# Optimization experiments

Hardware: AMD Instinct MI355X
Metric: run time of the kernel (lower is better)

## Reference

```python
import jax, jax.numpy as jnp
import numpy as np

D_MODEL = 512
D_STATE = 16
D_INNER = 2 * D_MODEL  # expand_factor=2
IN_CH = 256
B_SZ, H_SZ, W_SZ = 4, 32, 32


def setup_inputs() -> dict:
    key = jax.random.key(0)
    ks = jax.random.split(key, 24)
    f = jax.random.normal
    inp = {}
    inp["x_V"] = f(ks[0], (B_SZ, IN_CH, H_SZ, W_SZ), jnp.float32)
    inp["x_I"] = f(ks[1], (B_SZ, IN_CH, H_SZ, W_SZ), jnp.float32)
    # channel_reduce: 1x1 conv + BN (inference stats)
    inp["conv_red_w"] = f(ks[2], (D_MODEL, IN_CH), jnp.float32) * 0.05
    inp["bn_red_g"] = jnp.ones((D_MODEL,), jnp.float32)
    inp["bn_red_b"] = jnp.zeros((D_MODEL,), jnp.float32)
    inp["bn_red_m"] = jnp.zeros((D_MODEL,), jnp.float32)
    inp["bn_red_v"] = jnp.ones((D_MODEL,), jnp.float32)
    # channel_restore: 1x1 conv + BN
    inp["conv_res_w"] = f(ks[3], (IN_CH, D_MODEL), jnp.float32) * 0.05
    inp["bn_res_g"] = jnp.ones((IN_CH,), jnp.float32)
    inp["bn_res_b"] = jnp.zeros((IN_CH,), jnp.float32)
    inp["bn_res_m"] = jnp.zeros((IN_CH,), jnp.float32)
    inp["bn_res_v"] = jnp.ones((IN_CH,), jnp.float32)
    # lambda_predictor convs (1x1 on pooled features == linear)
    inp["lam_w1"] = f(ks[4], (D_MODEL // 4, D_MODEL * 2), jnp.float32) * 0.05
    inp["lam_b1"] = jnp.zeros((D_MODEL // 4,), jnp.float32)
    inp["lam_w2"] = f(ks[5], (2, D_MODEL // 4), jnp.float32) * 0.05
    inp["lam_b2"] = jnp.zeros((2,), jnp.float32)
    # two SimplifiedMamba2Blocks
    for i, p in enumerate(["V", "I"]):
        kk = jax.random.split(ks[6 + i], 6)
        inp[p + "_in_w"] = f(kk[0], (2 * D_INNER, D_MODEL), jnp.float32) * 0.03
        inp[p + "_out_w"] = f(kk[1], (D_MODEL, D_INNER), jnp.float32) * 0.03
        # A = -exp(A_log) in (-1, -0.05): stable decay
        inp[p + "_A_log"] = jnp.log(jax.random.uniform(kk[2], (D_INNER, D_STATE), jnp.float32, 0.05, 0.95))
        inp[p + "_B"] = f(kk[3], (D_INNER, D_STATE), jnp.float32) * 0.05
        inp[p + "_C"] = jnp.full((D_INNER, D_STATE), 0.01, jnp.float32)
        inp[p + "_ln_g"] = jnp.ones((D_MODEL,), jnp.float32)
        inp[p + "_ln_b"] = jnp.zeros((D_MODEL,), jnp.float32)
    inp["gate"] = jnp.asarray(0.1, jnp.float32)
    return inp


def _bn(x, g, b, m, v):
    # x: (B,C,H,W); inference-mode batchnorm
    return (x - m[:, None, None]) / jnp.sqrt(v[:, None, None] + 1e-5) * g[:, None, None] + b[:, None, None]


def _conv1x1(x, w):
    return jnp.einsum('bchw,oc->bohw', x, w)


def _ssm_scan(x_ssm, A, Bm, Cm, reverse):
    # x_ssm: (B,L,I); A,Bm,Cm: (I,S)
    bsz = x_ssm.shape[0]
    h0 = jnp.zeros((bsz, A.shape[0], A.shape[1]), x_ssm.dtype)

    def step(h, xt):  # xt: (B,I)
        h = jnp.clip(h * A + xt[:, :, None] * Bm, -10.0, 10.0)
        return h, jnp.einsum('bis,is->bi', h, Cm)

    _, ys = jax.lax.scan(step, h0, jnp.swapaxes(x_ssm, 0, 1), reverse=reverse)
    return jnp.swapaxes(ys, 0, 1)  # (B,L,I), in original time order


def _mamba(x, ln_g, ln_b, in_w, out_w, A_log, Bm, Cm):
    # LayerNorm
    mu = jnp.mean(x, -1, keepdims=True)
    var = jnp.mean((x - mu) ** 2, -1, keepdims=True)
    xn = (x - mu) / jnp.sqrt(var + 1e-5) * ln_g + ln_b
    xp = xn @ in_w.T  # (B,L,2*I)
    x_ssm, gate = jnp.split(xp, 2, axis=-1)
    A = jnp.clip(-jnp.exp(A_log), -10.0, -0.01)
    yf = _ssm_scan(x_ssm, A, Bm, Cm, False)
    yb = _ssm_scan(x_ssm, A, Bm, Cm, True)
    out = 0.5 * (yf + yb) * jax.nn.silu(gate)
    return out @ out_w.T


def reference(x_V, x_I, conv_red_w, bn_red_g, bn_red_b, bn_red_m, bn_red_v,
              conv_res_w, bn_res_g, bn_res_b, bn_res_m, bn_res_v,
              lam_w1, lam_b1, lam_w2, lam_b2,
              V_in_w, V_out_w, V_A_log, V_B, V_C, V_ln_g, V_ln_b,
              I_in_w, I_out_w, I_A_log, I_B, I_C, I_ln_g, I_ln_b, gate):
    B, _, H, W = x_V.shape
    xVr = jax.nn.relu(_bn(_conv1x1(x_V, conv_red_w), bn_red_g, bn_red_b, bn_red_m, bn_red_v))
    xIr = jax.nn.relu(_bn(_conv1x1(x_I, conv_red_w), bn_red_g, bn_red_b, bn_red_m, bn_red_v))
    # same spatial size -> adaptive pooling and [:B] slicing are identities
    conc = jnp.concatenate([xVr, xIr], axis=1)  # (B, 2*d_model, H, W)

    def lam(c):
        p = jnp.mean(c, axis=(2, 3))  # global avg pool -> (B, 2*d_model)
        h1 = jax.nn.relu(p @ lam_w1.T + lam_b1)
        return jax.nn.softmax(h1 @ lam_w2.T + lam_b2, axis=-1)  # (B,2)

    lamV = lam(conc)
    lamI = lam(conc)

    seq_V = jnp.swapaxes(xVr.reshape(B, D_MODEL, H * W), 1, 2)  # (B,L,D)
    seq_I = jnp.swapaxes(xIr.reshape(B, D_MODEL, H * W), 1, 2)

    outV_std = _mamba(seq_V, V_ln_g, V_ln_b, V_in_w, V_out_w, V_A_log, V_B, V_C)
    outI_std = _mamba(seq_I, I_ln_g, I_ln_b, I_in_w, I_out_w, I_A_log, I_B, I_C)
    outV_cross = _mamba(seq_V, V_ln_g, V_ln_b, V_in_w, V_out_w, V_A_log, jax.lax.stop_gradient(I_B), V_C)
    outI_cross = _mamba(seq_I, I_ln_g, I_ln_b, I_in_w, I_out_w, I_A_log, jax.lax.stop_gradient(V_B), I_C)

    outV = lamV[:, 0][:, None, None] * outV_std + lamV[:, 1][:, None, None] * outV_cross
    outI = lamI[:, 0][:, None, None] * outI_std + lamI[:, 1][:, None, None] * outI_cross

    featV = jnp.swapaxes(outV, 1, 2).reshape(B, D_MODEL, H, W)
    featI = jnp.swapaxes(outI, 1, 2).reshape(B, D_MODEL, H, W)
    featV = _bn(_conv1x1(featV, conv_res_w), bn_res_g, bn_res_b, bn_res_m, bn_res_v)
    featI = _bn(_conv1x1(featI, conv_res_w), bn_res_g, bn_res_b, bn_res_m, bn_res_v)

    g = jax.nn.sigmoid(gate)
    return (x_V + g * featV, x_I + g * featI)
```

## Files before the change

### kernel.cpp

```cpp
#include <hip/hip_runtime.h>
#include <hip/hip_bf16.h>
#include <math.h>

#define L_SZ 1024
#define DM   512
#define DI   1024
#define NS   16
#define CH   256

typedef float4 f4;
typedef __attribute__((ext_vector_type(8))) short short8;
typedef __attribute__((ext_vector_type(4))) float f32x4;

__device__ __forceinline__ float bf2f(ushort u) {
    union { unsigned int i; float f; } x; x.i = ((unsigned int)u) << 16; return x.f;
}
__device__ __forceinline__ ushort f2bf(float f) {
    union { float f; unsigned int i; } x; x.f = f;
    unsigned int r = x.i + 0x7FFFu + ((x.i >> 16) & 1u);
    return (ushort)(r >> 16);
}
__device__ __forceinline__ uint pkbf(float a, float b) {
    union { __hip_bfloat162 h; uint u; } c;
    c.h = __float22bfloat162_rn(make_float2(a, b));
    return c.u;
}

#define GLOAD16(gp, lp) \
  __builtin_amdgcn_global_load_lds((const __attribute__((address_space(1))) void*)(gp), \
                                   (__attribute__((address_space(3))) void*)(lp), 16, 0, 0)

__global__ __launch_bounds__(256) void k_cast_all(
    const float* __restrict__ s0, const float* __restrict__ s1,
    const float* __restrict__ s2, const float* __restrict__ s3,
    const float* __restrict__ s4, const float* __restrict__ s5,
    ushort* __restrict__ d0, ushort* __restrict__ d1,
    ushort* __restrict__ d2, ushort* __restrict__ d3,
    ushort* __restrict__ d4, ushort* __restrict__ d5)
{
    const int bid = blockIdx.x;
    const float* s; ushort* d; int rel;
    if      (bid < 128)  { s = s0; d = d0; rel = bid; }
    else if (bid < 256)  { s = s1; d = d1; rel = bid - 128; }
    else if (bid < 1280) { s = s2; d = d2; rel = bid - 256; }
    else if (bid < 2304) { s = s3; d = d3; rel = bid - 1280; }
    else if (bid < 2816) { s = s4; d = d4; rel = bid - 2304; }
    else                 { s = s5; d = d5; rel = bid - 2816; }
    const int i = rel * 256 + threadIdx.x;
    f4 v = ((const f4*)s)[i];
    ushort4 o;
    o.x = f2bf(v.x); o.y = f2bf(v.y); o.z = f2bf(v.z); o.w = f2bf(v.w);
    ((ushort4*)d)[i] = o;
}

__global__ __launch_bounds__(256) void k_xt(const float* __restrict__ xv,
                                            const float* __restrict__ xi,
                                            ushort* __restrict__ xtv,
                                            ushort* __restrict__ xti)
{
    __shared__ float tile[32][36];
    const int t = threadIdx.x;
    const int l0 = blockIdx.x * 32, c0 = blockIdx.y * 32;
    const int b = blockIdx.z & 3, st = blockIdx.z >> 2;
    const float* x = st ? xi : xv;
    ushort* xt = st ? xti : xtv;
    {
        int cc = t >> 3, ll4 = (t & 7) << 2;
        f4 v = *(const f4*)(x + ((size_t)(b * CH + c0 + cc)) * L_SZ + l0 + ll4);
        tile[cc][ll4 + 0] = v.x; tile[cc][ll4 + 1] = v.y;
        tile[cc][ll4 + 2] = v.z; tile[cc][ll4 + 3] = v.w;
    }
    __syncthreads();
    {
        int ll = t >> 3, cc4 = (t & 7) << 2;
        ushort4 o;
        o.x = f2bf(tile[cc4 + 0][ll]); o.y = f2bf(tile[cc4 + 1][ll]);
        o.z = f2bf(tile[cc4 + 2][ll]); o.w = f2bf(tile[cc4 + 3][ll]);
        *(ushort4*)(xt + ((size_t)(b * L_SZ + l0 + ll)) * CH + c0 + cc4) = o;
    }
}

template<int MODE, int BM, int BN>
__global__ __launch_bounds__(256) void k_gemm(
    const ushort* __restrict__ A0, const ushort* __restrict__ A1,
    const ushort* __restrict__ B0, const ushort* __restrict__ B1,
    int K,
    float* __restrict__ o0, float* __restrict__ o1,
    ushort* __restrict__ ob0, ushort* __restrict__ ob1,
    ushort* __restrict__ sb0, ushort* __restrict__ sb1,
    const float* __restrict__ pg, const float* __restrict__ pb,
    const float* __restrict__ pm, const float* __restrict__ pv,
    const float* __restrict__ x0, const float* __restrict__ x1,
    const float* __restrict__ gate, float* __restrict__ pp)
{
    constexpr int MT   = BM / 32;
    constexpr int NT   = BN / 32;
    constexpr int ASEG = BM / 16;
    constexpr int NSEG = (BM + BN) / 16;
    constexpr int SPW  = NSEG / 4;
    __shared__ __align__(16) ushort Sl[(BM + BN) * 32];
    const int t = threadIdx.x;
    const int wv = t >> 6, lane = t & 63;
    const int n0 = blockIdx.x * BN, m0 = blockIdx.y * BM;
    const int st = blockIdx.z;
    const ushort* Ap = st ? A1 : A0;
    const ushort* Bp = st ? B1 : B0;
    const int wm = wv >> 1, wn = wv & 1;
    const int lrow = lane & 15, q = lane >> 4;
    f32x4 acc[MT][NT];
    #pragma unroll
    for (int a_ = 0; a_ < MT; ++a_)
        #pragma unroll
        for (int b_ = 0; b_ < NT; ++b_)
            acc[a_][b_] = (f32x4){0.f, 0.f, 0.f, 0.f};
    const int srow = lane >> 2;
    const int skk  = (((lane & 3) ^ ((lane >> 3) & 3)) << 3);
    const int koff = ((q ^ ((lrow >> 1) & 3)) << 3);
    for (int k0 = 0; k0 < K; k0 += 32) {
        #pragma unroll
        for (int s2 = 0; s2 < SPW; ++s2) {
            const int seg = wv * SPW + s2;
            const int grow = (seg < ASEG) ? (m0 + seg * 16 + srow)
                                          : (n0 + (seg - ASEG) * 16 + srow);
            const ushort* src = (seg < ASEG) ? Ap : Bp;
            GLOAD16(src + (size_t)grow * K + k0 + skk, &Sl[seg * 512]);
        }
        __syncthreads();
        short8 af[MT], bfr[NT];
        #pragma unroll
        for (int mt = 0; mt < MT; ++mt)
            af[mt] = *(const short8*)&Sl[(wm * (MT * 16) + mt * 16 + lrow) * 32 + koff];
        #pragma unroll
        for (int nt = 0; nt < NT; ++nt)
            bfr[nt] = *(const short8*)&Sl[(BM + wn * (NT * 16) + nt * 16 + lrow) * 32 + koff];
        #pragma unroll
        for (int mt = 0; mt < MT; ++mt)
            #pragma unroll
            for (int nt = 0; nt < NT; ++nt)
                acc[mt][nt] = __builtin_amdgcn_mfma_f32_16x16x32_bf16(af[mt], bfr[nt], acc[mt][nt], 0, 0, 0);
        __syncthreads();
    }
    if (MODE == 0) {
        float* op = st ? o1 : o0;
        const int b = m0 >> 10;
        #pragma unroll
        for (int nt = 0; nt < NT; ++nt) {
            const int gn = n0 + wn * (NT * 16) + nt * 16 + lrow;
            const float s  = pg[gn] * rsqrtf(pv[gn] + 1e-5f);
            const float sh = pb[gn] - pm[gn] * s;
            float psum = 0.f;
            #pragma unroll
            for (int mt = 0; mt < MT; ++mt) {
                const int gm = m0 + wm * (MT * 16) + mt * 16 + q * 4;
                #pragma unroll
                for (int r = 0; r < 4; ++r) {
                    const float v = fmaxf(fmaf(acc[mt][nt][r], s, sh), 0.f);
                    op[(size_t)(gm + r) * DM + gn] = v;
                    psum += v;
                }
            }
            psum += __shfl_xor(psum, 16, 64);
            psum += __shfl_xor(psum, 32, 64);
            if (q == 0)
                atomicAdd(pp + (b * 1024 + st * 512 + gn), psum * (1.0f / 1024.0f));
        }
    } else if (MODE == 1) {
        const bool isx = (n0 < 1024);
        ushort* xp = st ? ob1 : ob0;
        ushort* sp = st ? sb1 : sb0;
        #pragma unroll
        for (int nt = 0; nt < NT; ++nt) {
            const int gn = n0 + wn * (NT * 16) + nt * 16 + lrow;
            #pragma unroll
            for (int mt = 0; mt < MT; ++mt) {
                const int gm = m0 + wm * (MT * 16) + mt * 16 + q * 4;
                if (isx) {
                    const uint u01 = pkbf(acc[mt][nt][0], acc[mt][nt][1]);
                    const uint u23 = pkbf(acc[mt][nt][2], acc[mt][nt][3]);
                    ushort* bp = xp + (size_t)gm * DI + gn;
                    bp[0]      = (ushort)u01;
                    bp[DI]     = (ushort)(u01 >> 16);
                    bp[2 * DI] = (ushort)u23;
                    bp[3 * DI] = (ushort)(u23 >> 16);
                } else {
                    float sv[4];
                    #pragma unroll
                    for (int r = 0; r < 4; ++r) {
                        const float v = acc[mt][nt][r];
                        sv[r] = v / (1.f + __expf(-v));
                    }
                    const uint u01 = pkbf(sv[0], sv[1]);
                    const uint u23 = pkbf(sv[2], sv[3]);
                    ushort* bp = sp + (size_t)gm * DI + gn - 1024;
                    bp[0]      = (ushort)u01;
                    bp[DI]     = (ushort)(u01 >> 16);
                    bp[2 * DI] = (ushort)u23;
                    bp[3 * DI] = (ushort)(u23 >> 16);
                }
            }
        }
    } else if (MODE == 2) {
        ushort* fp_ = st ? ob1 : ob0;
        #pragma unroll
        for (int nt = 0; nt < NT; ++nt) {
            const int gn = n0 + wn * (NT * 16) + nt * 16 + lrow;
            #pragma unroll
            for (int mt = 0; mt < MT; ++mt) {
                const int gm = m0 + wm * (MT * 16) + mt * 16 + q * 4;
                const uint u01 = pkbf(acc[mt][nt][0], acc[mt][nt][1]);
                const uint u23 = pkbf(acc[mt][nt][2], acc[mt][nt][3]);
                ushort* bp = fp_ + (size_t)gm * DM + gn;
                bp[0]      = (ushort)u01;
                bp[DM]     = (ushort)(u01 >> 16);
                bp[2 * DM] = (ushort)u23;
                bp[3 * DM] = (ushort)(u23 >> 16);
            }
        }
    } else {
        const float* xin = st ? x1 : x0;
        float* op = st ? o1 : o0;
        const float g = 1.f / (1.f + __expf(-gate[0]));
        #pragma unroll
        for (int nt = 0; nt < NT; ++nt) {
            const int gn = n0 + wn * (NT * 16) + nt * 16 + lrow;
            const float s  = pg[gn] * rsqrtf(pv[gn] + 1e-5f);
            const float sh = pb[gn] - pm[gn] * s;
            #pragma unroll
            for (int mt = 0; mt < MT; ++mt) {
                const int gmb = m0 + wm * (MT * 16) + mt * 16 + q * 4;
                const int b = gmb >> 10, l = gmb & 1023;
                const size_t off = ((size_t)(b * CH + gn)) * L_SZ + l;
                f4 xi = *(const f4*)(xin + off);
                f4 o;
                o.x = xi.x + g * fmaf(acc[mt][nt][0], s, sh);
                o.y = xi.y + g * fmaf(acc[mt][nt][1], s, sh);
                o.z = xi.z + g * fmaf(acc[mt][nt][2], s, sh);
                o.w = xi.w + g * fmaf(acc[mt][nt][3], s, sh);
                *(f4*)(op + off) = o;
            }
        }
    }
}

__global__ __launch_bounds__(256) void k_lam1(
    const float* __restrict__ p, const float* __restrict__ w1,
    const float* __restrict__ b1, float* __restrict__ h1)
{
    const int t = threadIdx.x, lane = t & 63, wv = t >> 6;
    const int idx = blockIdx.x * 4 + wv;
    const int b = idx >> 7, j = idx & 127;
    const float* pb = p + b * 1024;
    const float* wr = w1 + j * 1024;
    float s = 0.f;
    #pragma unroll
    for (int k = 0; k < 16; ++k)
        s = fmaf(pb[lane + k * 64], wr[lane + k * 64], s);
    #pragma unroll
    for (int off = 1; off < 64; off <<= 1) s += __shfl_xor(s, off, 64);
    if (lane == 0) h1[idx] = fmaxf(s + b1[j], 0.f);
}

__global__ __launch_bounds__(512) void k_lam2(
    const float* __restrict__ h1, const float* __restrict__ w2,
    const float* __restrict__ b2, float* __restrict__ lam)
{
    __shared__ float lg[8];
    const int t = threadIdx.x, lane = t & 63, wv = t >> 6;
    const int b = wv >> 1, k = wv & 1;
    const float* hb = h1 + b * 128;
    const float* wr = w2 + k * 128;
    float s = fmaf(hb[lane], wr[lane], hb[lane + 64] * wr[lane + 64]);
    #pragma unroll
    for (int off = 1; off < 64; off <<= 1) s += __shfl_xor(s, off, 64);
    if (lane == 0) lg[wv] = s + b2[k];
    __syncthreads();
    if (t < 4) {
        const float a0 = lg[t * 2], a1 = lg[t * 2 + 1];
        const float m  = fmaxf(a0, a1);
        const float e0 = __expf(a0 - m), e1 = __expf(a1 - m);
        const float inv = 1.f / (e0 + e1);
        lam[t * 2 + 0] = e0 * inv;
        lam[t * 2 + 1] = e1 * inv;
    }
}

__global__ __launch_bounds__(128) void k_ln(
    const float* __restrict__ seq0, const float* __restrict__ seq1,
    const float* __restrict__ g0, const float* __restrict__ b0,
    const float* __restrict__ g1, const float* __restrict__ b1,
    ushort* __restrict__ ln0, ushort* __restrict__ ln1)
{
    __shared__ float red[2][2];
    const int row = blockIdx.x, st = blockIdx.y;
    const float* seq = st ? seq1 : seq0;
    const float* gg  = st ? g1 : g0;
    const float* bb  = st ? b1 : b0;
    ushort* ln = st ? ln1 : ln0;
    const int t = threadIdx.x, wv2 = t >> 6, lane = t & 63;
    f4 v = *(const f4*)(seq + (size_t)row * DM + t * 4);
    float s = v.x + v.y + v.z + v.w;
    float ss = v.x * v.x + v.y * v.y + v.z * v.z + v.w * v.w;
    #pragma unroll
    for (int off = 1; off < 64; off <<= 1) {
        s += __shfl_xor(s, off, 64); ss += __shfl_xor(ss, off, 64);
    }
    if (lane == 0) { red[wv2][0] = s; red[wv2][1] = ss; }
    __syncthreads();
    const float tot = red[0][0] + red[1][0], tot2 = red[0][1] + red[1][1];
    const float mu = tot * (1.f / 512.f);
    const float rstd = rsqrtf(tot2 * (1.f / 512.f) - mu * mu + 1e-5f);
    f4 gv = *(const f4*)(gg + t * 4);
    f4 bv = *(const f4*)(bb + t * 4);
    ushort4 o;
    o.x = f2bf(fmaf((v.x - mu) * rstd, gv.x, bv.x));
    o.y = f2bf(fmaf((v.y - mu) * rstd, gv.y, bv.y));
    o.z = f2bf(fmaf((v.z - mu) * rstd, gv.z, bv.z));
    o.w = f2bf(fmaf((v.w - mu) * rstd, gv.w, bv.w));
    *(ushort4*)(ln + (size_t)row * DM + t * 4) = o;
}

__global__ __launch_bounds__(256) void k_scan(
    const ushort* __restrict__ xsV, const ushort* __restrict__ xsI,
    const float* __restrict__ VA, const float* __restrict__ VB,
    const float* __restrict__ VC, const float* __restrict__ IA,
    const float* __restrict__ IB, const float* __restrict__ IC,
    const float* __restrict__ lam,
    ushort* __restrict__ accfV, ushort* __restrict__ accbV,
    ushort* __restrict__ accfI, ushort* __restrict__ accbI)
{
    __shared__ __align__(16) ushort xbuf[2][32][128];
    const int t = threadIdx.x;
    const int lane = t & 63, wv = t >> 6;
    const int shalf = t & 1;
    const int il = t >> 1;
    const int b = blockIdx.y;
    const int cfg = blockIdx.z & 3, j = blockIdx.z >> 2;
    const int st = cfg >> 1, dir = cfg & 1;
    const ushort* xs = st ? xsI : xsV;
    const float* Alog = st ? IA : VA;
    const float* Cm   = st ? IC : VC;
    const float* Bown = st ? IB : VB;
    const float* Both = st ? VB : IB;
    ushort* out = st ? (dir ? accbI : accfI) : (dir ? accbV : accfV);
    const float lam0 = lam[b * 2 + 0], lam1 = lam[b * 2 + 1];
    float a[8], w[8], g[8];
    const int base = (blockIdx.x * 128 + il) * NS + shalf * 8;
    #pragma unroll
    for (int s = 0; s < 8; ++s) {
        a[s] = fminf(fmaxf(-__expf(Alog[base + s]), -10.f), -0.01f);
        w[s] = Cm[base + s] * fmaf(lam0, Bown[base + s], lam1 * Both[base + s]);
        g[s] = 0.f;
    }
    const ushort* xbase = xs + (size_t)b * L_SZ * DI + blockIdx.x * 128;
    ushort* op = out + (size_t)b * L_SZ * DI + blockIdx.x * 128 + il;
    const int c0    = j == 0 ? 0 : 4 * j - 3;
    const int ncha  = j == 0 ? 4 : 7;
    const int nwarm = j == 0 ? 0 : 3;
    const int lrow  = wv * 4 + (lane >> 4);
    const int lcol8 = (lane & 15) << 3;
    {
        #pragma unroll
        for (int is = 0; is < 2; ++is) {
            const int lr = (c0 << 5) + is * 16 + lrow;
            const int l  = dir ? (1023 - lr) : lr;
            GLOAD16(xbase + (size_t)l * DI + lcol8, &xbuf[0][is * 16 + wv * 4][0]);
        }
    }
    __syncthreads();
    for (int ci = 0; ci < ncha; ++ci) {
        const int cidx = c0 + ci;
        const int buf = ci & 1;
        if (ci + 1 < ncha) {
            #pragma unroll
            for (int is = 0; is < 2; ++is) {
                const int lr = ((cidx + 1) << 5) + is * 16 + lrow;
                const int l  = dir ? (1023 - lr) : lr;
                GLOAD16(xbase + (size_t)l * DI + lcol8, &xbuf[buf ^ 1][is * 16 + wv * 4][0]);
            }
        }
        if (ci < nwarm) {
            #pragma unroll
            for (int n = 0; n < 32; ++n) {
                const float x = bf2f(xbuf[buf][n][il]);
                #pragma unroll
                for (int s = 0; s < 8; ++s)
                    g[s] = fmaf(a[s], g[s], x);
            }
        } else {
            #pragma unroll
            for (int n = 0; n < 32; ++n) {
                const float x = bf2f(xbuf[buf][n][il]);
                float y0 = 0.f, y1 = 0.f;
                #pragma unroll
                for (int s = 0; s < 8; s += 2) {
                    g[s]     = fmaf(a[s],     g[s],     x);
                    y0       = fmaf(g[s],     w[s],     y0);
                    g[s + 1] = fmaf(a[s + 1], g[s + 1], x);
                    y1       = fmaf(g[s + 1], w[s + 1], y1);
                }
                float z = y0 + y1;
                z += __shfl_xor(z, 1, 64);
                if (shalf == 0) {
                    const int lp = (cidx << 5) + n;
                    const int l  = dir ? (1023 - lp) : lp;
                    op[(size_t)l * DI] = f2bf(z);
                }
            }
        }
        __syncthreads();
    }
}

__global__ __launch_bounds__(256) void k_combine(
    const ushort* __restrict__ fV, const ushort* __restrict__ bV,
    const ushort* __restrict__ fI, const ushort* __restrict__ bI,
    const ushort* __restrict__ sgV, const ushort* __restrict__ sgI,
    ushort* __restrict__ yV, ushort* __restrict__ yI)
{
    const int st = blockIdx.y;
    const size_t i = (size_t)blockIdx.x * 256 + threadIdx.x;
    const ushort4 f = ((const ushort4*)(st ? fI : fV))[i];
    const ushort4 g = ((const ushort4*)(st ? bI : bV))[i];
    const ushort4 s = ((const ushort4*)(st ? sgI : sgV))[i];
    ushort4 o;
    o.x = f2bf((bf2f(f.x) + bf2f(g.x)) * 0.5f * bf2f(s.x));
    o.y = f2bf((bf2f(f.y) + bf2f(g.y)) * 0.5f * bf2f(s.y));
    o.z = f2bf((bf2f(f.z) + bf2f(g.z)) * 0.5f * bf2f(s.z));
    o.w = f2bf((bf2f(f.w) + bf2f(g.w)) * 0.5f * bf2f(s.w));
    ((ushort4*)(st ? yI : yV))[i] = o;
}

extern "C" void kernel_launch(void* const* d_in, const int* in_sizes, int n_in,
                              void* d_out, int out_size, void* d_ws, size_t ws_size,
                              hipStream_t stream)
{
    const float* xV       = (const float*)d_in[0];
    const float* xI       = (const float*)d_in[1];
    const float* convredw = (const float*)d_in[2];
    const float* bnredg   = (const float*)d_in[3];
    const float* bnredb   = (const float*)d_in[4];
    const float* bnredm   = (const float*)d_in[5];
    const float* bnredv   = (const float*)d_in[6];
    const float* convresw = (const float*)d_in[7];
    const float* bnresg   = (const float*)d_in[8];
    const float* bnresb   = (const float*)d_in[9];
    const float* bnresm   = (const float*)d_in[10];
    const float* bnresv   = (const float*)d_in[11];
    const float* lamw1    = (const float*)d_in[12];
    const float* lamb1    = (const float*)d_in[13];
    const float* lamw2    = (const float*)d_in[14];
    const float* lamb2    = (const float*)d_in[15];
    const float* Vinw     = (const float*)d_in[16];
    const float* Voutw    = (const float*)d_in[17];
    const float* VAlog    = (const float*)d_in[18];
    const float* VB       = (const float*)d_in[19];
    const float* VC       = (const float*)d_in[20];
    const float* Vlng     = (const float*)d_in[21];
    const float* Vlnb     = (const float*)d_in[22];
    const float* Iinw     = (const float*)d_in[23];
    const float* Ioutw    = (const float*)d_in[24];
    const float* IAlog    = (const float*)d_in[25];
    const float* IB       = (const float*)d_in[26];
    const float* IC       = (const float*)d_in[27];
    const float* Ilng     = (const float*)d_in[28];
    const float* Ilnb     = (const float*)d_in[29];
    const float* gate     = (const float*)d_in[30];

    char* W = (char*)d_ws;
    const size_t MB = 1048576;
    float*  seqV  = (float*)(W + 0);
    float*  seqI  = (float*)(W + 8  * MB);
    float*  p     = (float*)(W + 16 * MB);
    float*  lam   = (float*)(W + 16 * MB + 16384);
    float*  h1    = (float*)(W + 16 * MB + 32768);
    ushort* sgV   = (ushort*)(W + 17 * MB);
    ushort* sgI   = (ushort*)(W + 25 * MB);
    ushort* accfV = (ushort*)(W + 33 * MB);
    ushort* accbV = (ushort*)(W + 41 * MB);
    ushort* accfI = (ushort*)(W + 49 * MB);
    ushort* accbI = (ushort*)(W + 57 * MB);
    ushort* wred  = (ushort*)(W + 65 * MB);
    ushort* wres  = (ushort*)(W + 65 * MB + 262144);
    ushort* winV  = (ushort*)(W + 66 * MB);
    ushort* winI  = (ushort*)(W + 68 * MB);
    ushort* woutV = (ushort*)(W + 70 * MB);
    ushort* woutI = (ushort*)(W + 71 * MB);
    ushort* xtV   = (ushort*)(W + 72 * MB);
    ushort* xtI   = (ushort*)(W + 74 * MB);
    ushort* lnV   = (ushort*)(W + 76 * MB);
    ushort* lnI   = (ushort*)(W + 80 * MB);
    ushort* xsV   = (ushort*)(W + 84 * MB);
    ushort* xsI   = (ushort*)(W + 92 * MB);
    ushort* yV    = xsV;
    ushort* yI    = xsI;
    ushort* featV = (ushort*)seqV;
    ushort* featI = (ushort*)seqI;
    float*  outp  = (float*)d_out;

    k_cast_all<<<dim3(3328), 256, 0, stream>>>(
        convredw, convresw, Vinw, Iinw, Voutw, Ioutw,
        wred, wres, winV, winI, woutV, woutI);
    k_xt<<<dim3(32, 8, 8), 256, 0, stream>>>(xV, xI, xtV, xtI);
    hipMemsetAsync(p, 0, 4096 * sizeof(float), stream);
    k_gemm<0, 128, 64><<<dim3(8, 32, 2), 256, 0, stream>>>(xtV, xtI, wred, wred, 256,
        seqV, seqI, nullptr, nullptr, nullptr, nullptr,
        bnredg, bnredb, bnredm, bnredv, nullptr, nullptr, nullptr, p);
    k_lam1<<<128, 256, 0, stream>>>(p, lamw1, lamb1, h1);
    k_lam2<<<1, 512, 0, stream>>>(h1, lamw2, lamb2, lam);
    k_ln<<<dim3(4096, 2), 128, 0, stream>>>(seqV, seqI, Vlng, Vlnb, Ilng, Ilnb, lnV, lnI);
    k_gemm<1, 128, 128><<<dim3(16, 32, 2), 256, 0, stream>>>(lnV, lnI, winV, winI, 512,
        nullptr, nullptr, xsV, xsI, sgV, sgI,
        nullptr, nullptr, nullptr, nullptr, nullptr, nullptr, nullptr, nullptr);
    k_scan<<<dim3(8, 4, 32), 256, 0, stream>>>(xsV, xsI, VAlog, VB, VC,
        IAlog, IB, IC, lam, accfV, accbV, accfI, accbI);
    k_combine<<<dim3(4096, 2), 256, 0, stream>>>(accfV, accbV, accfI, accbI,
        sgV, sgI, yV, yI);
    k_gemm<2, 128, 64><<<dim3(8, 32, 2), 256, 0, stream>>>(yV, yI, woutV, woutI, 1024,
        nullptr, nullptr, featV, featI, nullptr, nullptr,
        nullptr, nullptr, nullptr, nullptr, nullptr, nullptr, nullptr, nullptr);
    k_gemm<3, 64, 64><<<dim3(4, 64, 2), 256, 0, stream>>>(featV, featI, wres, wres, 512,
        outp, outp + 1048576, nullptr, nullptr, nullptr, nullptr,
        bnresg, bnresb, bnresm, bnresv, xV, xI, gate, nullptr);
}
```

Before: 265.6 us.

## Fuse prep kernels, store reduced sequence in bf16, merge lambda kernels

```diff
diff --git a/kernel.cpp b/kernel.cpp
--- a/kernel.cpp
+++ b/kernel.cpp
@@ -10,6 +10,7 @@
 
 typedef float4 f4;
 typedef __attribute__((ext_vector_type(8))) short short8;
+typedef __attribute__((ext_vector_type(8))) unsigned short u16x8;
 typedef __attribute__((ext_vector_type(4))) float f32x4;
 
 __device__ __forceinline__ float bf2f(ushort u) {
@@ -30,54 +31,64 @@
   __builtin_amdgcn_global_load_lds((const __attribute__((address_space(1))) void*)(gp), \
                                    (__attribute__((address_space(3))) void*)(lp), 16, 0, 0)
 
-__global__ __launch_bounds__(256) void k_cast_all(
+__global__ __launch_bounds__(256) void k_prep(
     const float* __restrict__ s0, const float* __restrict__ s1,
     const float* __restrict__ s2, const float* __restrict__ s3,
     const float* __restrict__ s4, const float* __restrict__ s5,
     ushort* __restrict__ d0, ushort* __restrict__ d1,
     ushort* __restrict__ d2, ushort* __restrict__ d3,
-    ushort* __restrict__ d4, ushort* __restrict__ d5)
-{
+    ushort* __restrict__ d4, ushort* __restrict__ d5,
+    const float* __restrict__ xv, const float* __restrict__ xi,
+    ushort* __restrict__ xtv, ushort* __restrict__ xti,
+    float* __restrict__ p, unsigned int* __restrict__ cnt)
+{
+    __shared__ float tile[32][36];
     const int bid = blockIdx.x;
-    const float* s; ushort* d; int rel;
-    if      (bid < 128)  { s = s0; d = d0; rel = bid; }
-    else if (bid < 256)  { s = s1; d = d1; rel = bid - 128; }
-    else if (bid < 1280) { s = s2; d = d2; rel = bid - 256; }
-    else if (bid < 2304) { s = s3; d = d3; rel = bid - 1280; }
-    else if (bid < 2816) { s = s4; d = d4; rel = bid - 2304; }
-    else                 { s = s5; d = d5; rel = bid - 2816; }
-    const int i = rel * 256 + threadIdx.x;
-    f4 v = ((const f4*)s)[i];
-    ushort4 o;
-    o.x = f2bf(v.x); o.y = f2bf(v.y); o.z = f2bf(v.z); o.w = f2bf(v.w);
-    ((ushort4*)d)[i] = o;
-}
-
-__global__ __launch_bounds__(256) void k_xt(const float* __restrict__ xv,
-                                            const float* __restrict__ xi,
-                                            ushort* __restrict__ xtv,
-                                            ushort* __restrict__ xti)
-{
-    __shared__ float tile[32][36];
     const int t = threadIdx.x;
-    const int l0 = blockIdx.x * 32, c0 = blockIdx.y * 32;
-    const int b = blockIdx.z & 3, st = blockIdx.z >> 2;
-    const float* x = st ? xi : xv;
-    ushort* xt = st ? xti : xtv;
-    {
-        int cc = t >> 3, ll4 = (t & 7) << 2;
-        f4 v = *(const f4*)(x + ((size_t)(b * CH + c0 + cc)) * L_SZ + l0 + ll4);
-        tile[cc][ll4 + 0] = v.x; tile[cc][ll4 + 1] = v.y;
-        tile[cc][ll4 + 2] = v.z; tile[cc][ll4 + 3] = v.w;
-    }
-    __syncthreads();
-    {
-        int ll = t >> 3, cc4 = (t & 7) << 2;
+    if (bid < 3328) {
+        const float* s; ushort* d; int rel;
+        if      (bid < 128)  { s = s0; d = d0; rel = bid; }
+        else if (bid < 256)  { s = s1; d = d1; rel = bid - 128; }
+        else if (bid < 1280) { s = s2; d = d2; rel = bid - 256; }
+        else if (bid < 2304) { s = s3; d = d3; rel = bid - 1280; }
+        else if (bid < 2816) { s = s4; d = d4; rel = bid - 2304; }
+        else                 { s = s5; d = d5; rel = bid - 2816; }
+        const int i = rel * 256 + t;
+        f4 v = ((const f4*)s)[i];
         ushort4 o;
-        o.x = f2bf(tile[cc4 + 0][ll]); o.y = f2bf(tile[cc4 + 1][ll]);
-        o.z = f2bf(tile[cc4 + 2][ll]); o.w = f2bf(tile[cc4 + 3][ll]);
-        *(ushort4*)(xt + ((size_t)(b * L_SZ + l0 + ll)) * CH + c0 + cc4) = o;
-    }
+        o.x = f2bf(v.x); o.y = f2bf(v.y); o.z = f2bf(v.z); o.w = f2bf(v.w);
+        ((ushort4*)d)[i] = o;
+        return;
+    }
+    if (bid < 5376) {
+        const int rel = bid - 3328;
+        const int l0 = (rel & 31) * 32, c0 = ((rel >> 5) & 7) * 32;
+        const int z = rel >> 8;
+        const int b = z & 3, st = z >> 2;
+        const float* x = st ? xi : xv;
+        ushort* xt = st ? xti : xtv;
+        {
+            int cc = t >> 3, ll4 = (t & 7) << 2;
+            f4 v = *(const f4*)(x + ((size_t)(b * CH + c0 + cc)) * L_SZ + l0 + ll4);
+            tile[cc][ll4 + 0] = v.x; tile[cc][ll4 + 1] = v.y;
+            tile[cc][ll4 + 2] = v.z; tile[cc][ll4 + 3] = v.w;
+        }
+        __syncthreads();
+        {
+            int ll = t >> 3, cc4 = (t & 7) << 2;
+            ushort4 o;
+            o.x = f2bf(tile[cc4 + 0][ll]); o.y = f2bf(tile[cc4 + 1][ll]);
+            o.z = f2bf(tile[cc4 + 2][ll]); o.w = f2bf(tile[cc4 + 3][ll]);
+            *(ushort4*)(xt + ((size_t)(b * L_SZ + l0 + ll)) * CH + c0 + cc4) = o;
+        }
+        return;
+    }
+    const f4 z4 = {0.f, 0.f, 0.f, 0.f};
+    ((f4*)p)[t]       = z4;
+    ((f4*)p)[t + 256] = z4;
+    ((f4*)p)[t + 512] = z4;
+    ((f4*)p)[t + 768] = z4;
+    if (t == 0) *cnt = 0u;
 }
 
 template<int MODE, int BM, int BN>
@@ -141,7 +152,7 @@
         __syncthreads();
     }
     if (MODE == 0) {
-        float* op = st ? o1 : o0;
+        ushort* sq = st ? ob1 : ob0;
         const int b = m0 >> 10;
         #pragma unroll
         for (int nt = 0; nt < NT; ++nt) {
@@ -152,12 +163,19 @@
             #pragma unroll
             for (int mt = 0; mt < MT; ++mt) {
                 const int gm = m0 + wm * (MT * 16) + mt * 16 + q * 4;
+                float v[4];
                 #pragma unroll
                 for (int r = 0; r < 4; ++r) {
-                    const float v = fmaxf(fmaf(acc[mt][nt][r], s, sh), 0.f);
-                    op[(size_t)(gm + r) * DM + gn] = v;
-                    psum += v;
+                    v[r] = fmaxf(fmaf(acc[mt][nt][r], s, sh), 0.f);
+                    psum += v[r];
                 }
+                const uint u01 = pkbf(v[0], v[1]);
+                const uint u23 = pkbf(v[2], v[3]);
+                ushort* bp = sq + (size_t)gm * DM + gn;
+                bp[0]      = (ushort)u01;
+                bp[DM]     = (ushort)(u01 >> 16);
+                bp[2 * DM] = (ushort)u23;
+                bp[3 * DM] = (ushort)(u23 >> 16);
             }
             psum += __shfl_xor(psum, 16, 64);
             psum += __shfl_xor(psum, 32, 64);
@@ -242,10 +260,14 @@
     }
 }
 
-__global__ __launch_bounds__(256) void k_lam1(
+__global__ __launch_bounds__(256) void k_lam(
     const float* __restrict__ p, const float* __restrict__ w1,
-    const float* __restrict__ b1, float* __restrict__ h1)
-{
+    const float* __restrict__ b1, const float* __restrict__ w2,
+    const float* __restrict__ b2, float* __restrict__ h1,
+    float* __restrict__ lam, unsigned int* __restrict__ cnt)
+{
+    __shared__ float lsm[8];
+    __shared__ unsigned int tick;
     const int t = threadIdx.x, lane = t & 63, wv = t >> 6;
     const int idx = blockIdx.x * 4 + wv;
     const int b = idx >> 7, j = idx & 127;
@@ -258,24 +280,28 @@
     #pragma unroll
     for (int off = 1; off < 64; off <<= 1) s += __shfl_xor(s, off, 64);
     if (lane == 0) h1[idx] = fmaxf(s + b1[j], 0.f);
-}
-
-__global__ __launch_bounds__(512) void k_lam2(
-    const float* __restrict__ h1, const float* __restrict__ w2,
-    const float* __restrict__ b2, float* __restrict__ lam)
-{
-    __shared__ float lg[8];
-    const int t = threadIdx.x, lane = t & 63, wv = t >> 6;
-    const int b = wv >> 1, k = wv & 1;
-    const float* hb = h1 + b * 128;
-    const float* wr = w2 + k * 128;
-    float s = fmaf(hb[lane], wr[lane], hb[lane + 64] * wr[lane + 64]);
-    #pragma unroll
-    for (int off = 1; off < 64; off <<= 1) s += __shfl_xor(s, off, 64);
-    if (lane == 0) lg[wv] = s + b2[k];
+    __threadfence();
+    __syncthreads();
+    if (t == 0) tick = atomicAdd(cnt, 1u);
+    __syncthreads();
+    if (tick != 127u) return;
+    __threadfence();
+    {
+        const int g32 = t >> 5, l32 = t & 31;
+        const int bb = g32 >> 1, kk = g32 & 1;
+        const float* hb = h1 + bb * 128;
+        const float* wr2 = w2 + kk * 128;
+        float ss = 0.f;
+        #pragma unroll
+        for (int u = 0; u < 4; ++u)
+            ss = fmaf(hb[l32 + u * 32], wr2[l32 + u * 32], ss);
+        #pragma unroll
+        for (int off = 1; off < 32; off <<= 1) ss += __shfl_xor(ss, off, 64);
+        if (l32 == 0) lsm[g32] = ss + b2[kk];
+    }
     __syncthreads();
     if (t < 4) {
-        const float a0 = lg[t * 2], a1 = lg[t * 2 + 1];
+        const float a0 = lsm[t * 2], a1 = lsm[t * 2 + 1];
         const float m  = fmaxf(a0, a1);
         const float e0 = __expf(a0 - m), e1 = __expf(a1 - m);
         const float inv = 1.f / (e0 + e1);
@@ -284,39 +310,48 @@
     }
 }
 
-__global__ __launch_bounds__(128) void k_ln(
-    const float* __restrict__ seq0, const float* __restrict__ seq1,
+__global__ __launch_bounds__(256) void k_ln(
+    const ushort* __restrict__ seq0, const ushort* __restrict__ seq1,
     const float* __restrict__ g0, const float* __restrict__ b0,
     const float* __restrict__ g1, const float* __restrict__ b1,
     ushort* __restrict__ ln0, ushort* __restrict__ ln1)
 {
-    __shared__ float red[2][2];
-    const int row = blockIdx.x, st = blockIdx.y;
-    const float* seq = st ? seq1 : seq0;
+    const int t = threadIdx.x, lane = t & 63, wv = t >> 6;
+    const int row = blockIdx.x * 4 + wv, st = blockIdx.y;
+    const ushort* seq = st ? seq1 : seq0;
     const float* gg  = st ? g1 : g0;
     const float* bb  = st ? b1 : b0;
     ushort* ln = st ? ln1 : ln0;
-    const int t = threadIdx.x, wv2 = t >> 6, lane = t & 63;
-    f4 v = *(const f4*)(seq + (size_t)row * DM + t * 4);
-    float s = v.x + v.y + v.z + v.w;
-    float ss = v.x * v.x + v.y * v.y + v.z * v.z + v.w * v.w;
+    const u16x8 v = *(const u16x8*)(seq + (size_t)row * DM + lane * 8);
+    float f[8];
+    float s = 0.f, ss = 0.f;
+    #pragma unroll
+    for (int i = 0; i < 8; ++i) {
+        f[i] = bf2f(v[i]);
+        s += f[i];
+        ss = fmaf(f[i], f[i], ss);
+    }
     #pragma unroll
     for (int off = 1; off < 64; off <<= 1) {
         s += __shfl_xor(s, off, 64); ss += __shfl_xor(ss, off, 64);
     }
-    if (lane == 0) { red[wv2][0] = s; red[wv2][1] = ss; }
-    __syncthreads();
-    const float tot = red[0][0] + red[1][0], tot2 = red[0][1] + red[1][1];
-    const float mu = tot * (1.f / 512.f);
-    const float rstd = rsqrtf(tot2 * (1.f / 512.f) - mu * mu + 1e-5f);
-    f4 gv = *(const f4*)(gg + t * 4);
-    f4 bv = *(const f4*)(bb + t * 4);
-    ushort4 o;
-    o.x = f2bf(fmaf((v.x - mu) * rstd, gv.x, bv.x));
-    o.y = f2bf(fmaf((v.y - mu) * rstd, gv.y, bv.y));
-    o.z = f2bf(fmaf((v.z - mu) * rstd, gv.z, bv.z));
-    o.w = f2bf(fmaf((v.w - mu) * rstd, gv.w, bv.w));
-    *(ushort4*)(ln + (size_t)row * DM + t * 4) = o;
+    const float mu = s * (1.f / 512.f);
+    const float rstd = rsqrtf(ss * (1.f / 512.f) - mu * mu + 1e-5f);
+    const f4 gv0 = *(const f4*)(gg + lane * 8);
+    const f4 gv1 = *(const f4*)(gg + lane * 8 + 4);
+    const f4 bv0 = *(const f4*)(bb + lane * 8);
+    const f4 bv1 = *(const f4*)(bb + lane * 8 + 4);
+    const float gvv[8] = {gv0.x, gv0.y, gv0.z, gv0.w, gv1.x, gv1.y, gv1.z, gv1.w};
+    const float bvv[8] = {bv0.x, bv0.y, bv0.z, bv0.w, bv1.x, bv1.y, bv1.z, bv1.w};
+    u16x8 o;
+    #pragma unroll
+    for (int i = 0; i < 8; i += 2) {
+        const uint u = pkbf(fmaf((f[i]     - mu) * rstd, gvv[i],     bvv[i]),
+                            fmaf((f[i + 1] - mu) * rstd, gvv[i + 1], bvv[i + 1]));
+        o[i]     = (ushort)u;
+        o[i + 1] = (ushort)(u >> 16);
+    }
+    *(u16x8*)(ln + (size_t)row * DM + lane * 8) = o;
 }
 
 __global__ __launch_bounds__(256) void k_scan(
@@ -348,7 +383,7 @@
     #pragma unroll
     for (int s = 0; s < 8; ++s) {
         a[s] = fminf(fmaxf(-__expf(Alog[base + s]), -10.f), -0.01f);
-        w[s] = Cm[base + s] * fmaf(lam0, Bown[base + s], lam1 * Both[base + s]);
+        w[s] = 0.5f * Cm[base + s] * fmaf(lam0, Bown[base + s], lam1 * Both[base + s]);
         g[s] = 0.f;
     }
     const ushort* xbase = xs + (size_t)b * L_SZ * DI + blockIdx.x * 128;
@@ -423,10 +458,10 @@
     const ushort4 g = ((const ushort4*)(st ? bI : bV))[i];
     const ushort4 s = ((const ushort4*)(st ? sgI : sgV))[i];
     ushort4 o;
-    o.x = f2bf((bf2f(f.x) + bf2f(g.x)) * 0.5f * bf2f(s.x));
-    o.y = f2bf((bf2f(f.y) + bf2f(g.y)) * 0.5f * bf2f(s.y));
-    o.z = f2bf((bf2f(f.z) + bf2f(g.z)) * 0.5f * bf2f(s.z));
-    o.w = f2bf((bf2f(f.w) + bf2f(g.w)) * 0.5f * bf2f(s.w));
+    o.x = f2bf((bf2f(f.x) + bf2f(g.x)) * bf2f(s.x));
+    o.y = f2bf((bf2f(f.y) + bf2f(g.y)) * bf2f(s.y));
+    o.z = f2bf((bf2f(f.z) + bf2f(g.z)) * bf2f(s.z));
+    o.w = f2bf((bf2f(f.w) + bf2f(g.w)) * bf2f(s.w));
     ((ushort4*)(st ? yI : yV))[i] = o;
 }
 
@@ -468,11 +503,12 @@
 
     char* W = (char*)d_ws;
     const size_t MB = 1048576;
-    float*  seqV  = (float*)(W + 0);
-    float*  seqI  = (float*)(W + 8  * MB);
-    float*  p     = (float*)(W + 16 * MB);
-    float*  lam   = (float*)(W + 16 * MB + 16384);
-    float*  h1    = (float*)(W + 16 * MB + 32768);
+    ushort* seqV  = (ushort*)(W + 0);
+    ushort* seqI  = (ushort*)(W + 4  * MB);
+    float*  p     = (float*)(W + 8 * MB);
+    float*  lam   = (float*)(W + 8 * MB + 16384);
+    float*  h1    = (float*)(W + 8 * MB + 32768);
+    unsigned int* cnt = (unsigned int*)(W + 8 * MB + 49152);
     ushort* sgV   = (ushort*)(W + 17 * MB);
     ushort* sgI   = (ushort*)(W + 25 * MB);
     ushort* accfV = (ushort*)(W + 33 * MB);
@@ -493,21 +529,19 @@
     ushort* xsI   = (ushort*)(W + 92 * MB);
     ushort* yV    = xsV;
     ushort* yI    = xsI;
-    ushort* featV = (ushort*)seqV;
-    ushort* featI = (ushort*)seqI;
+    ushort* featV = seqV;
+    ushort* featI = seqI;
     float*  outp  = (float*)d_out;
 
-    k_cast_all<<<dim3(3328), 256, 0, stream>>>(
+    k_prep<<<dim3(5377), 256, 0, stream>>>(
         convredw, convresw, Vinw, Iinw, Voutw, Ioutw,
-        wred, wres, winV, winI, woutV, woutI);
-    k_xt<<<dim3(32, 8, 8), 256, 0, stream>>>(xV, xI, xtV, xtI);
-    hipMemsetAsync(p, 0, 4096 * sizeof(float), stream);
+        wred, wres, winV, winI, woutV, woutI,
+        xV, xI, xtV, xtI, p, cnt);
     k_gemm<0, 128, 64><<<dim3(8, 32, 2), 256, 0, stream>>>(xtV, xtI, wred, wred, 256,
-        seqV, seqI, nullptr, nullptr, nullptr, nullptr,
+        nullptr, nullptr, seqV, seqI, nullptr, nullptr,
         bnredg, bnredb, bnredm, bnredv, nullptr, nullptr, nullptr, p);
-    k_lam1<<<128, 256, 0, stream>>>(p, lamw1, lamb1, h1);
-    k_lam2<<<1, 512, 0, stream>>>(h1, lamw2, lamb2, lam);
-    k_ln<<<dim3(4096, 2), 128, 0, stream>>>(seqV, seqI, Vlng, Vlnb, Ilng, Ilnb, lnV, lnI);
+    k_lam<<<128, 256, 0, stream>>>(p, lamw1, lamb1, lamw2, lamb2, h1, lam, cnt);
+    k_ln<<<dim3(1024, 2), 256, 0, stream>>>(seqV, seqI, Vlng, Vlnb, Ilng, Ilnb, lnV, lnI);
     k_gemm<1, 128, 128><<<dim3(16, 32, 2), 256, 0, stream>>>(lnV, lnI, winV, winI, 512,
         nullptr, nullptr, xsV, xsI, sgV, sgI,
         nullptr, nullptr, nullptr, nullptr, nullptr, nullptr, nullptr, nullptr);
```

Result: no change. 268.1 us (+0.9%).
